# Performance work log

Hardware: AMD Instinct MI355X
Metric: run time of the kernel (lower is better)

The kernel has to match this reference:

```python
import jax, jax.numpy as jnp
import numpy as np
import jax.scipy.linalg as jsl

N_SAMPLES = 100000
N_COMPONENTS = 64
N_FEATURES = 32
LOW, HIGH = -0.1, 0.1


def setup_inputs() -> dict:
    key = jax.random.key(0)
    k_x, k_mu = jax.random.split(key)
    X = jax.random.normal(k_x, (N_SAMPLES, N_FEATURES), dtype=jnp.float32)
    means = jax.random.uniform(k_mu, (N_COMPONENTS, N_FEATURES),
                               minval=LOW, maxval=HIGH, dtype=jnp.float32)
    # torch init: stack of tril(eye(D)) == identity for each component
    eye = jnp.eye(N_FEATURES, dtype=jnp.float32)
    scale_tril = jnp.tile(eye[None, :, :], (N_COMPONENTS, 1, 1))
    log_weights = jnp.zeros((N_COMPONENTS,), dtype=jnp.float32)
    return {"X": X, "means": means, "scale_tril": scale_tril,
            "log_weights": log_weights}


def reference(X, means, scale_tril, log_weights):
    N, D = X.shape
    LOG_2PI = jnp.log(jnp.asarray(2.0 * np.pi, dtype=X.dtype))

    def comp_log_prob(mu, L):
        # MVN log-prob via triangular whitening (matches torch MVN(scale_tril=L))
        diff = (X - mu).T                     # [D, N]
        z = jsl.solve_triangular(L, diff, lower=True)  # [D, N]
        maha = jnp.sum(z * z, axis=0)          # [N]
        half_logdet = jnp.sum(jnp.log(jnp.diagonal(L)))
        return -0.5 * (D * LOG_2PI + maha) - half_logdet  # [N]

    logp = jax.vmap(comp_log_prob)(means, scale_tril)  # [K, N]

    # E-step: responsibilities (raw exp, as in the original; no logsumexp)
    weights = jax.nn.softmax(log_weights)              # [K]
    unnorm = weights[:, None] * jnp.exp(logp)          # [K, N]
    resp = unnorm / jnp.sum(unnorm, axis=0, keepdims=True)  # [K, N]

    # M-step: note torch's F.log_softmax(log_weights[k], dim=-1) on a 0-d
    # tensor is identically 0 (softmax of a single element), so it is omitted.
    log_likelihood = jnp.sum(resp * logp, axis=0)      # [N]
    return -jnp.mean(log_likelihood)
```

## Files before the change

### kernel.cpp

```cpp
#include <hip/hip_runtime.h>
#include <math.h>

#define NS 100000
#define NC 64
#define ND 32
#define NK 576
#define NBLK ((NS + 255) / 256)
#define QBYTES (NC * NK * 2)
#define NCPB 8
#define LOG2PI 1.8378770664093453f

typedef __attribute__((ext_vector_type(8))) __bf16 bf16x8;
typedef __attribute__((ext_vector_type(8))) float  floatx8;
typedef __attribute__((ext_vector_type(4))) float  floatx4;



template<int I, int Q>
__device__ __forceinline__ void load_row(const floatx4* ls4, floatx4 (&rb)[8]) {
    if constexpr (Q <= I / 4) {
        rb[Q] = ls4[I * 8 + Q];
        load_row<I, Q + 1>(ls4, rb);
    }
}

template<int I, int L>
__device__ __forceinline__ void fchain(const floatx4 (&rb)[8], const float (&a)[ND], float& s) {
    if constexpr (L < I) {
        s = fmaf(-rb[L / 4][L % 4], a[L], s);
        fchain<I, L + 1>(rb, a, s);
    }
}

template<int I>
__device__ __forceinline__ void fsub2(const floatx4* ls4, float (&a)[ND], int j) {
    if constexpr (I < ND) {
        floatx4 rb[8];
        load_row<I, 0>(ls4, rb);
        float s = (I == j) ? 1.0f : 0.0f;
        fchain<I, 0>(rb, a, s);
        float v = s / rb[I / 4][I % 4];
        a[I] = (I < j) ? 0.0f : v;
        fsub2<I + 1>(ls4, a, j);
    }
}

template<int Q>
__device__ __forceinline__ void store_ac(float* acrow, const float (&a)[ND]) {
    if constexpr (Q < 8) {
        floatx4 t;
        t[0] = a[4 * Q + 0]; t[1] = a[4 * Q + 1];
        t[2] = a[4 * Q + 2]; t[3] = a[4 * Q + 3];
        *(floatx4*)(acrow + 4 * Q) = t;
        store_ac<Q + 1>(acrow, a);
    }
}

template<int JJ>
__device__ __forceinline__ void qpack(bf16x8& v, const float* Pc, const float* bbc,
                                      int t, int quad) {
    if constexpr (JJ < 8) {
        int u = quad * 8 + JJ;
        float val;
        if (t == 0)       val = -0.5f * Pc[u * 32 + u];
        else if (t < 16)  val = -Pc[u * 32 + ((u + t) & 31)];
        else if (t == 16) val = (u < 16) ? -Pc[u * 32 + u + 16] : bbc[u - 16];
        else              val = (u < 16) ? bbc[16 + u] : 0.0f;
        v[JJ] = (__bf16)val;
        qpack<JJ + 1>(v, Pc, bbc, t, quad);
    }
}

__launch_bounds__(512)
__global__ void gmm_setup(const float* __restrict__ means,
                          const float* __restrict__ scale_tril,
                          const float* __restrict__ log_weights,
                          __bf16* __restrict__ Qf,
                          float* __restrict__ lw,
                          float* __restrict__ kc) {
    __shared__ __align__(16) floatx4 LsP4[NCPB * 256];
    __shared__ __align__(16) float Ac[NCPB][32][36];
    __shared__ float mu_s[NCPB][32];
    __shared__ float bb_s[NCPB][32];

    const int tid  = threadIdx.x;
    const int b    = blockIdx.x;
    const int w    = tid >> 6;
    const int lane = tid & 63;

    {
        const floatx4* g4 = (const floatx4*)scale_tril + (size_t)b * 2048;
#pragma unroll
        for (int q = 0; q < 4; ++q)
            LsP4[q * 512 + tid] = g4[q * 512 + tid];
        if (tid < NCPB * 32)
            mu_s[tid >> 5][tid & 31] = means[(size_t)(b * NCPB + (tid >> 5)) * ND + (tid & 31)];
    }
    __syncthreads();

    const floatx4* ls4 = LsP4 + w * 256;
    if (lane < ND) {
        float a[ND];
        fsub2<0>(ls4, a, lane);
        store_ac<0>(&Ac[w][lane][0], a);
    }
    float hv = (lane < ND) ? logf(((const float*)LsP4)[w * 1024 + lane * 33]) : 0.0f;
#pragma unroll
    for (int off = 1; off < 64; off <<= 1) hv += __shfl_xor(hv, off);
    float hld = hv;
    __syncthreads();

    {
        int c = tid >> 6, half = (tid >> 5) & 1, i = tid & 31;
        const floatx4* rI4 = (const floatx4*)&Ac[c][i][0];
        float* Pc = (float*)LsP4 + c * 1024;
        for (int j16 = 0; j16 < 16; ++j16) {
            int j = half * 16 + j16;
            const floatx4* rJ4 = (const floatx4*)&Ac[c][j][0];
            float s = 0.0f;
#pragma unroll
            for (int q = 0; q < 8; ++q) {
                floatx4 x = rI4[q], y = rJ4[q];
                s = fmaf(x[0], y[0], s); s = fmaf(x[1], y[1], s);
                s = fmaf(x[2], y[2], s); s = fmaf(x[3], y[3], s);
            }
            Pc[i * 32 + j] = s;
        }
    }
    __syncthreads();

    const float* Pw = (const float*)LsP4 + w * 1024;
    float bbv = 0.0f;
    if (lane < ND) {
        for (int j = 0; j < ND; ++j) bbv = fmaf(Pw[lane * 32 + j], mu_s[w][j], bbv);
        bb_s[w][lane] = bbv;
    }
    float ccv = (lane < ND) ? mu_s[w][lane] * bbv : 0.0f;
#pragma unroll
    for (int off = 1; off < 64; off <<= 1) ccv += __shfl_xor(ccv, off);
    int comp = b * NCPB + w;
    if (lane == 0)
        kc[comp] = -0.5f * ccv - 16.0f * LOG2PI - hld;

    if (b == 0 && w == 0) {
        float x = log_weights[lane];
        float mx = x;
#pragma unroll
        for (int off = 1; off < 64; off <<= 1) mx = fmaxf(mx, __shfl_xor(mx, off));
        float e = __expf(x - mx);
#pragma unroll
        for (int off = 1; off < 64; off <<= 1) e += __shfl_xor(e, off);
        lw[lane] = x - mx - logf(e);
    }

    {
        int mt = comp >> 4, colk = comp & 15;
        const float* bbc = &bb_s[w][0];
        bf16x8* qdst = (bf16x8*)Qf;
        {
            int t = lane >> 2, quad = lane & 3;
            bf16x8 v;
            qpack<0>(v, Pw, bbc, t, quad);
            qdst[(size_t)(mt * 18 + t) * 64 + quad * 16 + colk] = v;
        }
        if (lane < 8) {
            int cl2 = 64 + lane;
            int t = cl2 >> 2, quad = cl2 & 3;
            bf16x8 v;
            qpack<0>(v, Pw, bbc, t, quad);
            qdst[(size_t)(mt * 18 + t) * 64 + quad * 16 + colk] = v;
        }
    }
}


template<int G>
__device__ __forceinline__ void fill_x(const float4* p, float (&xr)[ND], int quad) {
    if constexpr (G < 8) {
        float4 v = p[(G + 2 * quad) & 7];
        xr[4 * G + 0] = v.x; xr[4 * G + 1] = v.y;
        xr[4 * G + 2] = v.z; xr[4 * G + 3] = v.w;
        fill_x<G + 1>(p, xr, quad);
    }
}

template<int T, int JJ>
__device__ __forceinline__ void feat(const float (&xr0)[ND], const float (&xr1)[ND],
                                     int quad, floatx8& f0, floatx8& f1) {
    if constexpr (JJ < 8) {
        float a0, a1, b0, b1;
        if constexpr (T < 16) {
            a0 = xr0[JJ]; b0 = xr0[(JJ + T) & 31];
            a1 = xr1[JJ]; b1 = xr1[(JJ + T) & 31];
        } else if constexpr (T == 16) {
            a0 = (quad < 2) ? xr0[JJ] : 1.0f;  b0 = xr0[(JJ + 16) & 31];
            a1 = (quad < 2) ? xr1[JJ] : 1.0f;  b1 = xr1[(JJ + 16) & 31];
        } else {
            a0 = (quad < 2) ? xr0[(JJ + 16) & 31] : 0.0f; b0 = 1.0f;
            a1 = (quad < 2) ? xr1[(JJ + 16) & 31] : 0.0f; b1 = 1.0f;
        }
        f0[JJ] = a0 * b0;
        f1[JJ] = a1 * b1;
        feat<T, JJ + 1>(xr0, xr1, quad, f0, f1);
    }
}

template<int T, int MT>
__device__ __forceinline__ void mfma_step(const unsigned char* qlane, bf16x8 b0, bf16x8 b1,
                                          floatx4 (&A0)[4], floatx4 (&A1)[4]) {
    if constexpr (MT < 4) {
        bf16x8 af = *(const bf16x8*)(qlane + (MT * 18 + T) * 1024);
        A0[MT] = __builtin_amdgcn_mfma_f32_16x16x32_bf16(af, b0, A0[MT], 0, 0, 0);
        A1[MT] = __builtin_amdgcn_mfma_f32_16x16x32_bf16(af, b1, A1[MT], 0, 0, 0);
        mfma_step<T, MT + 1>(qlane, b0, b1, A0, A1);
    }
}

template<int T>
__device__ __forceinline__ void kloop(const unsigned char* qlane,
                                      const float (&xr0)[ND], const float (&xr1)[ND],
                                      int quad, floatx4 (&A0)[4], floatx4 (&A1)[4]) {
    if constexpr (T < 18) {
        floatx8 f0, f1;
        feat<T, 0>(xr0, xr1, quad, f0, f1);
        bf16x8 b0 = __builtin_convertvector(f0, bf16x8);
        bf16x8 b1 = __builtin_convertvector(f1, bf16x8);
        mfma_step<T, 0>(qlane, b0, b1, A0, A1);
        kloop<T + 1>(qlane, xr0, xr1, quad, A0, A1);
    }
}

template<int MT, int R>
__device__ __forceinline__ void epi_r(const floatx4 (&A0)[4], const floatx4 (&A1)[4],
                                      floatx4 lwv, floatx4 kcv,
                                      float& s0, float& w0, float& s1, float& w1) {
    if constexpr (R < 4) {
        float lp0 = A0[MT][R] + kcv[R];
        float e0 = __expf(lp0 + lwv[R]);
        s0 += e0; w0 = fmaf(e0, lp0, w0);
        float lp1 = A1[MT][R] + kcv[R];
        float e1 = __expf(lp1 + lwv[R]);
        s1 += e1; w1 = fmaf(e1, lp1, w1);
        epi_r<MT, R + 1>(A0, A1, lwv, kcv, s0, w0, s1, w1);
    }
}

template<int MT>
__device__ __forceinline__ void epi(const float* lw_s, const float* kc_s, int quad,
                                    const floatx4 (&A0)[4], const floatx4 (&A1)[4],
                                    float& s0, float& w0, float& s1, float& w1) {
    if constexpr (MT < 4) {
        floatx4 lwv = *(const floatx4*)&lw_s[MT * 16 + quad * 4];
        floatx4 kcv = *(const floatx4*)&kc_s[MT * 16 + quad * 4];
        epi_r<MT, 0>(A0, A1, lwv, kcv, s0, w0, s1, w1);
        epi<MT + 1>(lw_s, kc_s, quad, A0, A1, s0, w0, s1, w1);
    }
}

__device__ __forceinline__ float pair_ll(const float* __restrict__ X,
                                         const unsigned char* qlane,
                                         const float* lw_s, const float* kc_s,
                                         int n0, int quad) {
    int n1 = n0 + 16;
    int n0c = n0 < NS ? n0 : NS - 1;
    int n1c = n1 < NS ? n1 : NS - 1;

    float xr0[ND], xr1[ND];
    fill_x<0>((const float4*)(X + (size_t)n0c * ND), xr0, quad);
    fill_x<0>((const float4*)(X + (size_t)n1c * ND), xr1, quad);

    floatx4 A0[4], A1[4];
#pragma unroll
    for (int mt = 0; mt < 4; ++mt) {
        A0[mt] = (floatx4){0.f, 0.f, 0.f, 0.f};
        A1[mt] = (floatx4){0.f, 0.f, 0.f, 0.f};
    }

    kloop<0>(qlane, xr0, xr1, quad, A0, A1);

    float s0 = 0.f, w0 = 0.f, s1 = 0.f, w1 = 0.f;
    epi<0>(lw_s, kc_s, quad, A0, A1, s0, w0, s1, w1);

    s0 += __shfl_xor(s0, 16); s0 += __shfl_xor(s0, 32);
    w0 += __shfl_xor(w0, 16); w0 += __shfl_xor(w0, 32);
    s1 += __shfl_xor(s1, 16); s1 += __shfl_xor(s1, 32);
    w1 += __shfl_xor(w1, 16); w1 += __shfl_xor(w1, 32);

    float ll = 0.0f;
    ll += (n0 < NS) ? (w0 / s0) : 0.0f;
    ll += (n1 < NS) ? (w1 / s1) : 0.0f;
    return ll;
}

__launch_bounds__(256, 2)
__global__ void gmm_main(const float* __restrict__ X,
                         const __bf16* __restrict__ Qf,
                         const float* __restrict__ lw,
                         const float* __restrict__ kc,
                         float* __restrict__ pb) {
    __shared__ __align__(16) unsigned char qlds[QBYTES];
    __shared__ float lw_s[NC];
    __shared__ float kc_s[NC];
    __shared__ float partial[4];
    int tid = threadIdx.x;
    if (tid < NC) { lw_s[tid] = lw[tid]; kc_s[tid] = kc[tid]; }
    {
        const float4* gsrc = (const float4*)Qf;
        float4* ldst = (float4*)qlds;
#pragma unroll
        for (int i = 0; i < QBYTES / 16 / 256; ++i)
            ldst[i * 256 + tid] = gsrc[i * 256 + tid];
    }
    __syncthreads();

    const int lane = tid & 63;
    const int wave = tid >> 6;
    const int quad = lane >> 4;
    const unsigned char* qlane = qlds + lane * 16;

    int base = blockIdx.x * 256 + wave * 32 + (lane & 15);

    float ll = pair_ll(X, qlane, lw_s, kc_s, base, quad);
    asm volatile("" ::: "memory");
    ll      += pair_ll(X, qlane, lw_s, kc_s, base + 128, quad);

#pragma unroll
    for (int off = 1; off < 64; off <<= 1) ll += __shfl_xor(ll, off);
    if (lane == 0) partial[wave] = ll * 0.25f;
    __syncthreads();

    if (tid == 0)
        pb[blockIdx.x] = partial[0] + partial[1] + partial[2] + partial[3];
}

__global__ void gmm_reduce(const float* __restrict__ pb, float* __restrict__ out) {
    int tid = threadIdx.x;
    float s = 0.0f;
    for (int i = tid; i < NBLK; i += 256) s += pb[i];
#pragma unroll
    for (int off = 32; off > 0; off >>= 1) s += __shfl_down(s, off);
    __shared__ float wsum[4];
    if ((tid & 63) == 0) wsum[tid >> 6] = s;
    __syncthreads();
    if (tid == 0)
        out[0] = -(wsum[0] + wsum[1] + wsum[2] + wsum[3]) / (float)NS;
}

extern "C" void kernel_launch(void* const* d_in, const int* in_sizes, int n_in,
                              void* d_out, int out_size, void* d_ws, size_t ws_size,
                              hipStream_t stream) {
    const float* X           = (const float*)d_in[0];
    const float* means       = (const float*)d_in[1];
    const float* scale_tril  = (const float*)d_in[2];
    const float* log_weights = (const float*)d_in[3];

    char* ws = (char*)d_ws;
    __bf16* Qf = (__bf16*)ws;
    float*  lw = (float*)(ws + 73728);
    float*  kc = (float*)(ws + 73984);
    float*  pb = (float*)(ws + 74240);

    gmm_setup<<<NC / NCPB, 512, 0, stream>>>(means, scale_tril, log_weights, Qf, lw, kc);
    gmm_main<<<NBLK, 256, 0, stream>>>(X, Qf, lw, kc, pb);
    gmm_reduce<<<1, 256, 0, stream>>>(pb, (float*)d_out);
}
```

Measured before the change: 94.24 us.

## Split Q staging into two LDS halves to raise occupancy to three blocks

The shared-memory buffer for the quadratic-form matrix is halved: the first 32 components are staged and processed, then the second half is loaded into the same LDS buffer after a barrier and processed. This cuts LDS per block from about 72KB to 36KB, and launch bounds go from 2 to 3 blocks per CU to allow more concurrency. Accumulator arrays shrink from 4 to 2 tiles, lowering register pressure. The cost is a second global load and extra barriers, recomputing X features twice, and reloading X rows twice.

```diff
diff --git a/kernel.cpp b/kernel.cpp
--- a/kernel.cpp
+++ b/kernel.cpp
@@ -7,6 +7,7 @@
 #define NK 576
 #define NBLK ((NS + 255) / 256)
 #define QBYTES (NC * NK * 2)
+#define QHALF  (QBYTES / 2)
 #define NCPB 8
 #define LOG2PI 1.8378770664093453f
 
@@ -207,8 +208,8 @@
 
 template<int T, int MT>
 __device__ __forceinline__ void mfma_step(const unsigned char* qlane, bf16x8 b0, bf16x8 b1,
-                                          floatx4 (&A0)[4], floatx4 (&A1)[4]) {
-    if constexpr (MT < 4) {
+                                          floatx4 (&A0)[2], floatx4 (&A1)[2]) {
+    if constexpr (MT < 2) {
         bf16x8 af = *(const bf16x8*)(qlane + (MT * 18 + T) * 1024);
         A0[MT] = __builtin_amdgcn_mfma_f32_16x16x32_bf16(af, b0, A0[MT], 0, 0, 0);
         A1[MT] = __builtin_amdgcn_mfma_f32_16x16x32_bf16(af, b1, A1[MT], 0, 0, 0);
@@ -219,7 +220,7 @@
 template<int T>
 __device__ __forceinline__ void kloop(const unsigned char* qlane,
                                       const float (&xr0)[ND], const float (&xr1)[ND],
-                                      int quad, floatx4 (&A0)[4], floatx4 (&A1)[4]) {
+                                      int quad, floatx4 (&A0)[2], floatx4 (&A1)[2]) {
     if constexpr (T < 18) {
         floatx8 f0, f1;
         feat<T, 0>(xr0, xr1, quad, f0, f1);
@@ -231,7 +232,7 @@
 }
 
 template<int MT, int R>
-__device__ __forceinline__ void epi_r(const floatx4 (&A0)[4], const floatx4 (&A1)[4],
+__device__ __forceinline__ void epi_r(const floatx4 (&A0)[2], const floatx4 (&A1)[2],
                                       floatx4 lwv, floatx4 kcv,
                                       float& s0, float& w0, float& s1, float& w1) {
     if constexpr (R < 4) {
@@ -246,21 +247,22 @@
 }
 
 template<int MT>
-__device__ __forceinline__ void epi(const float* lw_s, const float* kc_s, int quad,
-                                    const floatx4 (&A0)[4], const floatx4 (&A1)[4],
+__device__ __forceinline__ void epi(const float* lw_h, const float* kc_h, int quad,
+                                    const floatx4 (&A0)[2], const floatx4 (&A1)[2],
                                     float& s0, float& w0, float& s1, float& w1) {
-    if constexpr (MT < 4) {
-        floatx4 lwv = *(const floatx4*)&lw_s[MT * 16 + quad * 4];
-        floatx4 kcv = *(const floatx4*)&kc_s[MT * 16 + quad * 4];
+    if constexpr (MT < 2) {
+        floatx4 lwv = *(const floatx4*)&lw_h[MT * 16 + quad * 4];
+        floatx4 kcv = *(const floatx4*)&kc_h[MT * 16 + quad * 4];
         epi_r<MT, 0>(A0, A1, lwv, kcv, s0, w0, s1, w1);
-        epi<MT + 1>(lw_s, kc_s, quad, A0, A1, s0, w0, s1, w1);
-    }
-}
-
-__device__ __forceinline__ float pair_ll(const float* __restrict__ X,
-                                         const unsigned char* qlane,
-                                         const float* lw_s, const float* kc_s,
-                                         int n0, int quad) {
+        epi<MT + 1>(lw_h, kc_h, quad, A0, A1, s0, w0, s1, w1);
+    }
+}
+
+__device__ __forceinline__ void pair_half(const float* __restrict__ X,
+                                          const unsigned char* qlane,
+                                          const float* lw_h, const float* kc_h,
+                                          int n0, int quad,
+                                          float& s0, float& w0, float& s1, float& w1) {
     int n1 = n0 + 16;
     int n0c = n0 < NS ? n0 : NS - 1;
     int n1c = n1 < NS ? n1 : NS - 1;
@@ -269,38 +271,26 @@
     fill_x<0>((const float4*)(X + (size_t)n0c * ND), xr0, quad);
     fill_x<0>((const float4*)(X + (size_t)n1c * ND), xr1, quad);
 
-    floatx4 A0[4], A1[4];
-#pragma unroll
-    for (int mt = 0; mt < 4; ++mt) {
+    floatx4 A0[2], A1[2];
+#pragma unroll
+    for (int mt = 0; mt < 2; ++mt) {
         A0[mt] = (floatx4){0.f, 0.f, 0.f, 0.f};
         A1[mt] = (floatx4){0.f, 0.f, 0.f, 0.f};
     }
 
     kloop<0>(qlane, xr0, xr1, quad, A0, A1);
-
-    float s0 = 0.f, w0 = 0.f, s1 = 0.f, w1 = 0.f;
-    epi<0>(lw_s, kc_s, quad, A0, A1, s0, w0, s1, w1);
-
-    s0 += __shfl_xor(s0, 16); s0 += __shfl_xor(s0, 32);
-    w0 += __shfl_xor(w0, 16); w0 += __shfl_xor(w0, 32);
-    s1 += __shfl_xor(s1, 16); s1 += __shfl_xor(s1, 32);
-    w1 += __shfl_xor(w1, 16); w1 += __shfl_xor(w1, 32);
-
-    float ll = 0.0f;
-    ll += (n0 < NS) ? (w0 / s0) : 0.0f;
-    ll += (n1 < NS) ? (w1 / s1) : 0.0f;
-    return ll;
-}
-
-__launch_bounds__(256, 2)
+    epi<0>(lw_h, kc_h, quad, A0, A1, s0, w0, s1, w1);
+}
+
+__launch_bounds__(256, 3)
 __global__ void gmm_main(const float* __restrict__ X,
                          const __bf16* __restrict__ Qf,
                          const float* __restrict__ lw,
                          const float* __restrict__ kc,
                          float* __restrict__ pb) {
-    __shared__ __align__(16) unsigned char qlds[QBYTES];
-    __shared__ float lw_s[NC];
-    __shared__ float kc_s[NC];
+    __shared__ __align__(16) unsigned char qlds[QHALF];
+    __shared__ __align__(16) float lw_s[NC];
+    __shared__ __align__(16) float kc_s[NC];
     __shared__ float partial[4];
     int tid = threadIdx.x;
     if (tid < NC) { lw_s[tid] = lw[tid]; kc_s[tid] = kc[tid]; }
@@ -308,7 +298,7 @@
         const float4* gsrc = (const float4*)Qf;
         float4* ldst = (float4*)qlds;
 #pragma unroll
-        for (int i = 0; i < QBYTES / 16 / 256; ++i)
+        for (int i = 0; i < QHALF / 16 / 256; ++i)
             ldst[i * 256 + tid] = gsrc[i * 256 + tid];
     }
     __syncthreads();
@@ -320,9 +310,41 @@
 
     int base = blockIdx.x * 256 + wave * 32 + (lane & 15);
 
-    float ll = pair_ll(X, qlane, lw_s, kc_s, base, quad);
+    float sA0 = 0.f, wA0 = 0.f, sA1 = 0.f, wA1 = 0.f;
+    float sB0 = 0.f, wB0 = 0.f, sB1 = 0.f, wB1 = 0.f;
+
+    pair_half(X, qlane, lw_s, kc_s, base, quad, sA0, wA0, sA1, wA1);
     asm volatile("" ::: "memory");
-    ll      += pair_ll(X, qlane, lw_s, kc_s, base + 128, quad);
+    pair_half(X, qlane, lw_s, kc_s, base + 128, quad, sB0, wB0, sB1, wB1);
+
+    __syncthreads();
+    {
+        const float4* gsrc = (const float4*)Qf + QHALF / 16;
+        float4* ldst = (float4*)qlds;
+#pragma unroll
+        for (int i = 0; i < QHALF / 16 / 256; ++i)
+            ldst[i * 256 + tid] = gsrc[i * 256 + tid];
+    }
+    __syncthreads();
+
+    pair_half(X, qlane, lw_s + 32, kc_s + 32, base, quad, sA0, wA0, sA1, wA1);
+    asm volatile("" ::: "memory");
+    pair_half(X, qlane, lw_s + 32, kc_s + 32, base + 128, quad, sB0, wB0, sB1, wB1);
+
+    sA0 += __shfl_xor(sA0, 16); sA0 += __shfl_xor(sA0, 32);
+    wA0 += __shfl_xor(wA0, 16); wA0 += __shfl_xor(wA0, 32);
+    sA1 += __shfl_xor(sA1, 16); sA1 += __shfl_xor(sA1, 32);
+    wA1 += __shfl_xor(wA1, 16); wA1 += __shfl_xor(wA1, 32);
+    sB0 += __shfl_xor(sB0, 16); sB0 += __shfl_xor(sB0, 32);
+    wB0 += __shfl_xor(wB0, 16); wB0 += __shfl_xor(wB0, 32);
+    sB1 += __shfl_xor(sB1, 16); sB1 += __shfl_xor(sB1, 32);
+    wB1 += __shfl_xor(wB1, 16); wB1 += __shfl_xor(wB1, 32);
+
+    float ll = 0.0f;
+    ll += (base       < NS) ? (wA0 / sA0) : 0.0f;
+    ll += (base + 16  < NS) ? (wA1 / sA1) : 0.0f;
+    ll += (base + 128 < NS) ? (wB0 / sB0) : 0.0f;
+    ll += (base + 144 < NS) ? (wB1 / sB1) : 0.0f;
 
 #pragma unroll
     for (int off = 1; off < 64; off <<= 1) ll += __shfl_xor(ll, off);
```

Result: slower. 98.93 us (+5.0%).
